# Performance work log

Measured on AMD Instinct MI355X. Metric: run time of the kernel, lower is better.

Reference implementation:

```python
import jax, jax.numpy as jnp
import numpy as np

NEG = -1000000.0  # mask fill value used by the torch module


def setup_inputs() -> dict:
    key = jax.random.key(0)
    kq, kk, kv, km = jax.random.split(key, 4)
    B, Q, K, D = 8, 2048, 2048, 128
    queries = jax.random.normal(kq, (B, Q, D), dtype=jnp.float32)
    keys = jax.random.normal(kk, (B, K, D), dtype=jnp.float32)
    values = jax.random.normal(kv, (B, K, D), dtype=jnp.float32)
    attntion_mask = jax.random.randint(km, (B, K), 0, 2, dtype=jnp.int32)
    return {"queries": queries, "keys": keys, "values": values,
            "attntion_mask": attntion_mask}


def reference(queries, keys, values, attntion_mask):
    d = queries.shape[-1]
    # scores: [B, Q, K]
    scores = jnp.einsum('bqd,bkd->bqk', queries, keys) / jnp.sqrt(
        jnp.asarray(d, dtype=queries.dtype))
    # 2D mask [B, K] broadcasts over the query axis (torch repeat_interleave)
    mask = attntion_mask.astype(bool)[:, None, :]  # [B, 1, K]
    scores = jnp.where(mask, scores, NEG)
    weights = jax.nn.softmax(scores, axis=-1)
    # dropout rate is 0.0 (eval mode) -> identity
    return jnp.einsum('bqk,bkv->bqv', weights, values)
```

## Files before the change

### kernel.cpp

```cpp
#include <hip/hip_runtime.h>
#include <stdint.h>

typedef __attribute__((ext_vector_type(8))) short short8;
typedef __attribute__((ext_vector_type(4))) float f32x4;

#define NB 8
#define NQ 2048
#define NK 2048
#define ND 128
#define SCALE 0.08838834764831845f
#define L2E   1.4426950408889634f
#define FMAXC 10.0f

__device__ __forceinline__ uint32_t pk_bf16(float a, float b) {
  uint32_t ua = __builtin_bit_cast(uint32_t, a);
  uint32_t ub = __builtin_bit_cast(uint32_t, b);
  ua += 0x7FFFu + ((ua >> 16) & 1u);
  ub += 0x7FFFu + ((ub >> 16) & 1u);
  return (ua >> 16) | (ub & 0xFFFF0000u);
}

__device__ __forceinline__ void dma16(const void* g, void* l) {
  __builtin_amdgcn_global_load_lds((const __attribute__((address_space(1))) void*)g,
                                   (__attribute__((address_space(3))) void*)l, 16, 0, 0);
}

__global__ __launch_bounds__(256) void compact_kernel(const int* __restrict__ maskm,
                                                      int* __restrict__ idxArr,
                                                      int* __restrict__ KcArr) {
  __shared__ int cnt;
  const int b = blockIdx.x;
  const int t = threadIdx.x;
  const int lane = t & 63;
  if (t == 0) cnt = 0;
  __syncthreads();
#pragma unroll
  for (int j = 0; j < 8; ++j) {
    int k = t * 8 + j;
    bool bit = maskm[b * NK + k] != 0;
    unsigned long long m = __ballot(bit);
    int pre = __popcll(m & ((1ull << lane) - 1ull));
    int tot = __popcll(m);
    int base = 0;
    if (lane == 0 && tot) base = atomicAdd(&cnt, tot);
    base = __shfl(base, 0);
    if (bit) idxArr[b * NK + base + pre] = k;
  }
  __syncthreads();
  int kc = cnt;
  for (int s = kc + t; s < NK; s += 256) idxArr[b * NK + s] = -1;
  if (t == 0) KcArr[b] = kc;
}

__global__ __launch_bounds__(256) void prep_kernel(const float* __restrict__ v,
                                                   const float* __restrict__ kin,
                                                   ushort* __restrict__ vt,
                                                   ushort* __restrict__ kb,
                                                   const int* __restrict__ idxArr) {
  const int t = threadIdx.x;
  const int bid = blockIdx.x;
  if (bid < 512) {
    __shared__ __align__(16) float tile[4096];
    char* sm = (char*)tile;
    const int b = bid >> 6;
    const int k0 = ((bid >> 1) & 31) << 6;
    const int d0 = (bid & 1) << 6;
#pragma unroll
    for (int i = 0; i < 4; ++i) {
      int id = i * 256 + t;
      int k = id >> 4, c = id & 15;
      int src = idxArr[b * NK + k0 + k];
      uint4 val; val.x = 0u; val.y = 0u; val.z = 0u; val.w = 0u;
      if (src >= 0) val = *(const uint4*)(v + (size_t)(b * NK + src) * ND + d0 + c * 4);
      *(uint4*)(sm + k * 256 + ((c ^ (k & 15)) * 16)) = val;
    }
    __syncthreads();
#pragma unroll
    for (int i = 0; i < 2; ++i) {
      int id = i * 256 + t;
      int d = id >> 3, kc = id & 7;
      uint32_t w[4];
#pragma unroll
      for (int jj = 0; jj < 4; ++jj) {
        int kA = kc * 8 + jj * 2, kB = kA + 1;
        float fa = *(const float*)(sm + kA * 256 + (((d >> 2) ^ (kA & 15)) * 16) + (d & 3) * 4);
        float fb = *(const float*)(sm + kB * 256 + (((d >> 2) ^ (kB & 15)) * 16) + (d & 3) * 4);
        w[jj] = pk_bf16(fa, fb);
      }
      uint4 o; o.x = w[0]; o.y = w[1]; o.z = w[2]; o.w = w[3];
      *(uint4*)(vt + (size_t)(b * ND + d0 + d) * NK + k0 + kc * 8) = o;
    }
  } else {
    int gs = (bid - 512) * 16 + (t >> 4);
    int src = idxArr[gs];
    int col = (t & 15) * 8;
    uint4 u; u.x = 0u; u.y = 0u; u.z = 0u; u.w = 0u;
    if (src >= 0) {
      int b2 = gs >> 11;
      const float* p = kin + (size_t)(b2 * NK + src) * ND + col;
      f32x4 a = *(const f32x4*)p;
      f32x4 c = *(const f32x4*)(p + 4);
      u.x = pk_bf16(a[0], a[1]); u.y = pk_bf16(a[2], a[3]);
      u.z = pk_bf16(c[0], c[1]); u.w = pk_bf16(c[2], c[3]);
    }
    *(uint4*)(kb + (size_t)gs * ND + col) = u;
  }
}

#define LDS_BYTES 73728
__global__ __launch_bounds__(256) void attn_kernel(const float* __restrict__ qm,
                                                   const ushort* __restrict__ kbm,
                                                   const ushort* __restrict__ vtm,
                                                   const int* __restrict__ KcArr,
                                                   ushort* __restrict__ opart,
                                                   float* __restrict__ lpart) {
  __shared__ __align__(16) char sm[LDS_BYTES];
  const int o   = blockIdx.x;
  const int bid = (o & 7) * 64 + (o >> 3);
  const int b   = bid >> 6;
  const int q0  = ((bid >> 1) & 31) << 6;
  const int spl = bid & 1;
  const int t = threadIdx.x;
  const int lane = t & 63;
  const int wave = t >> 6;
  const int r = lane & 15;
  const int quad = lane >> 4;
  const int half = wave >> 1;
  const int qg = wave & 1;

  const int Kc   = KcArr[b];
  const int n_it = (Kc + 127) >> 7;
  const int CH   = n_it << 5;

  uint32_t koff[4], voff[4];
#pragma unroll
  for (int j = 0; j < 4; ++j) {
    int i = wave * 4 + j;
    int rho = i * 4 + (lane >> 4);
    int ck = (lane & 15) ^ (rho & 15);
    int krow = (spl * 2 + (rho >> 5)) * CH + (rho & 31);
    koff[j] = (uint32_t)(b * NK + krow) * ND + ck * 8;
    int rv = i * 16 + (lane >> 2);
    int cv = (lane & 3) ^ (rv & 3);
    voff[j] = (uint32_t)(b * ND + (rv & 127)) * NK + (spl * 2 + (rv >> 7)) * CH + cv * 8;
  }

  short8 qf[2][4];
#pragma unroll
  for (int qt = 0; qt < 2; ++qt)
#pragma unroll
    for (int ks = 0; ks < 4; ++ks) {
      const float* p = qm + (size_t)(b * NQ + q0 + qg * 32 + qt * 16 + r) * ND + ks * 32 + quad * 8;
      f32x4 a = *(const f32x4*)p;
      f32x4 c = *(const f32x4*)(p + 4);
      uint4 u;
      u.x = pk_bf16(a[0], a[1]); u.y = pk_bf16(a[2], a[3]);
      u.z = pk_bf16(c[0], c[1]); u.w = pk_bf16(c[2], c[3]);
      qf[qt][ks] = __builtin_bit_cast(short8, u);
    }

  f32x4 oacc[2][8];
#pragma unroll
  for (int qt = 0; qt < 2; ++qt)
#pragma unroll
    for (int dt = 0; dt < 8; ++dt) oacc[qt][dt] = (f32x4){0.f, 0.f, 0.f, 0.f};
  float l_[2] = {0.f, 0.f};

  char* const pbase = sm + 65536 + wave * 2048;

  const int lim0 = Kc - (spl * 2 + half) * CH - quad * 4;

#pragma unroll
  for (int j = 0; j < 4; ++j) {
    dma16(kbm + koff[j], sm + wave * 4096 + j * 1024);
    dma16(vtm + voff[j], sm + 32768 + wave * 4096 + j * 1024);
  }

  for (int it = 0; it < n_it; ++it) {
    const int cur = it & 1;
    char* const kcur = sm + cur * 16384;
    char* const vcur = sm + 32768 + cur * 16384;
    char* const knxt = sm + (cur ^ 1) * 16384;
    char* const vnxt = sm + 32768 + (cur ^ 1) * 16384;

    __syncthreads();

    if (it < n_it - 1) {
      const uint32_t kadd = (uint32_t)(it + 1) * 32 * ND;
      const uint32_t vadd = (uint32_t)(it + 1) * 32;
#pragma unroll
      for (int j = 0; j < 4; ++j) {
        dma16(kbm + koff[j] + kadd, knxt + wave * 4096 + j * 1024);
        dma16(vtm + voff[j] + vadd, vnxt + wave * 4096 + j * 1024);
      }
    }

    short8 kf[2][4];
#pragma unroll
    for (int mt = 0; mt < 2; ++mt)
#pragma unroll
      for (int ks = 0; ks < 4; ++ks)
        kf[mt][ks] = *(const short8*)(kcur + half * 8192 + (mt * 16 + r) * 256 + (((ks * 4 + quad) ^ r) * 16));
    f32x4 st[2][2];
#pragma unroll
    for (int mt = 0; mt < 2; ++mt)
#pragma unroll
      for (int qt = 0; qt < 2; ++qt) {
        f32x4 acc = (f32x4){0.f, 0.f, 0.f, 0.f};
#pragma unroll
        for (int ks = 0; ks < 4; ++ks)
          acc = __builtin_amdgcn_mfma_f32_16x16x32_bf16(kf[mt][ks], qf[qt][ks], acc, 0, 0, 0);
        st[mt][qt] = acc;
      }

    const float C1 = SCALE * L2E;
    const float C2 = -FMAXC * L2E;
    const int rem = lim0 - it * 32;
#pragma unroll
    for (int qt = 0; qt < 2; ++qt) {
      float p[2][4]; float ps = 0.f;
#pragma unroll
      for (int mt = 0; mt < 2; ++mt) {
        const int rm = rem - mt * 16;
        float t0 = (rm > 0) ? fmaf(st[mt][qt][0], C1, C2) : -2.0e6f;
        float t1 = (rm > 1) ? fmaf(st[mt][qt][1], C1, C2) : -2.0e6f;
        float t2 = (rm > 2) ? fmaf(st[mt][qt][2], C1, C2) : -2.0e6f;
        float t3 = (rm > 3) ? fmaf(st[mt][qt][3], C1, C2) : -2.0e6f;
        p[mt][0] = exp2f(t0); p[mt][1] = exp2f(t1);
        p[mt][2] = exp2f(t2); p[mt][3] = exp2f(t3);
        ps += p[mt][0] + p[mt][1] + p[mt][2] + p[mt][3];
      }
      ps += __shfl_xor(ps, 16);
      ps += __shfl_xor(ps, 32);
      l_[qt] += ps;
#pragma unroll
      for (int mt = 0; mt < 2; ++mt) {
        uint2 w; w.x = pk_bf16(p[mt][0], p[mt][1]); w.y = pk_bf16(p[mt][2], p[mt][3]);
        *(uint2*)(pbase + (qt * 16 + r) * 64 + (((mt * 4 + quad) ^ (r & 6)) * 8)) = w;
      }
    }

    short8 pf[2];
#pragma unroll
    for (int qt = 0; qt < 2; ++qt)
      pf[qt] = *(const short8*)(pbase + (qt * 16 + r) * 64 + (((quad * 2) ^ (r & 6)) * 8));
#pragma unroll
    for (int dt = 0; dt < 8; ++dt) {
      short8 vf = *(const short8*)(vcur + half * 8192 + (dt * 16 + r) * 64 + ((quad ^ (r & 3)) * 16));
#pragma unroll
      for (int qt = 0; qt < 2; ++qt)
        oacc[qt][dt] = __builtin_amdgcn_mfma_f32_16x16x32_bf16(vf, pf[qt], oacc[qt][dt], 0, 0, 0);
    }
  }

  __syncthreads();
  float* xch = (float*)(sm + qg * 17408) + lane * 68;
  if (half == 1) {
    xch[0] = l_[0]; xch[1] = l_[1];
#pragma unroll
    for (int qt = 0; qt < 2; ++qt)
#pragma unroll
      for (int dt = 0; dt < 8; ++dt)
        *(f32x4*)(xch + 4 + (qt * 8 + dt) * 4) = oacc[qt][dt];
  }
  __syncthreads();
  if (half == 0) {
#pragma unroll
    for (int qt = 0; qt < 2; ++qt) {
      const int qrow = b * NQ + q0 + qg * 32 + qt * 16 + r;
      float lsum = l_[qt] + xch[qt];
      if (quad == 0) lpart[spl * NB * NQ + qrow] = lsum;
#pragma unroll
      for (int dt = 0; dt < 8; ++dt) {
        f32x4 o1 = *(const f32x4*)(xch + 4 + (qt * 8 + dt) * 4);
        f32x4 ov = oacc[qt][dt] + o1;
        uint2 w; w.x = pk_bf16(ov[0], ov[1]); w.y = pk_bf16(ov[2], ov[3]);
        *(uint2*)(opart + (size_t)spl * NB * NQ * ND + (size_t)qrow * ND + dt * 16 + quad * 4) = w;
      }
    }
  }
}

__global__ __launch_bounds__(256) void merge_kernel(const ushort* __restrict__ opart,
                                                    const float* __restrict__ lpart,
                                                    float* __restrict__ outm) {
  const int gid = blockIdx.x * 256 + threadIdx.x;
  const int row = gid >> 4;
  const int d0 = (gid & 15) << 3;
  const size_t off = (size_t)row * ND + d0;
  uint4 u0 = *(const uint4*)(opart + off);
  uint4 u1 = *(const uint4*)(opart + (size_t)NB * NQ * ND + off);
  float inv = 1.0f / (lpart[row] + lpart[NB * NQ + row]);
  f32x4 lo, hi;
  uint32_t w;
#define UP(u, dst0, dst1) w = (u); dst0 = __builtin_bit_cast(float, w << 16); \
                          dst1 = __builtin_bit_cast(float, w & 0xFFFF0000u);
  float a0,a1,b0,b1;
  UP(u0.x, a0, a1) UP(u1.x, b0, b1) lo[0] = (a0 + b0) * inv; lo[1] = (a1 + b1) * inv;
  UP(u0.y, a0, a1) UP(u1.y, b0, b1) lo[2] = (a0 + b0) * inv; lo[3] = (a1 + b1) * inv;
  UP(u0.z, a0, a1) UP(u1.z, b0, b1) hi[0] = (a0 + b0) * inv; hi[1] = (a1 + b1) * inv;
  UP(u0.w, a0, a1) UP(u1.w, b0, b1) hi[2] = (a0 + b0) * inv; hi[3] = (a1 + b1) * inv;
#undef UP
  *(f32x4*)(outm + off) = lo;
  *(f32x4*)(outm + off + 4) = hi;
}

extern "C" void kernel_launch(void* const* d_in, const int* in_sizes, int n_in,
                              void* d_out, int out_size, void* d_ws, size_t ws_size,
                              hipStream_t stream) {
  const float* q   = (const float*)d_in[0];
  const float* k   = (const float*)d_in[1];
  const float* v   = (const float*)d_in[2];
  const int*   msk = (const int*)d_in[3];
  float* out = (float*)d_out;
  ushort* kb = (ushort*)d_ws;
  ushort* vt = kb + (size_t)NB * NK * ND;
  ushort* op = vt + (size_t)NB * NK * ND;
  float*  lp = (float*)(op + 2 * (size_t)NB * NQ * ND);
  int* idxA  = (int*)(lp + 2 * (size_t)NB * NQ);
  int* kcA   = idxA + (size_t)NB * NK;

  compact_kernel<<<NB, 256, 0, stream>>>(msk, idxA, kcA);
  prep_kernel<<<1536, 256, 0, stream>>>(v, k, vt, kb, idxA);
  attn_kernel<<<512, 256, 0, stream>>>(q, kb, vt, kcA, op, lp);
  merge_kernel<<<1024, 256, 0, stream>>>(op, lp, out);
}
```

Baseline: 109.6 us.

## Fuse mask compaction into prep and load V fragments directly from global

New measurement: 113.4 us. +3.5%, slower.

```diff
diff --git a/kernel.cpp b/kernel.cpp
--- a/kernel.cpp
+++ b/kernel.cpp
@@ -25,51 +25,54 @@
                                    (__attribute__((address_space(3))) void*)l, 16, 0, 0);
 }
 
-__global__ __launch_bounds__(256) void compact_kernel(const int* __restrict__ maskm,
-                                                      int* __restrict__ idxArr,
-                                                      int* __restrict__ KcArr) {
-  __shared__ int cnt;
-  const int b = blockIdx.x;
-  const int t = threadIdx.x;
-  const int lane = t & 63;
-  if (t == 0) cnt = 0;
-  __syncthreads();
-#pragma unroll
-  for (int j = 0; j < 8; ++j) {
-    int k = t * 8 + j;
-    bool bit = maskm[b * NK + k] != 0;
-    unsigned long long m = __ballot(bit);
-    int pre = __popcll(m & ((1ull << lane) - 1ull));
-    int tot = __popcll(m);
-    int base = 0;
-    if (lane == 0 && tot) base = atomicAdd(&cnt, tot);
-    base = __shfl(base, 0);
-    if (bit) idxArr[b * NK + base + pre] = k;
-  }
-  __syncthreads();
-  int kc = cnt;
-  for (int s = kc + t; s < NK; s += 256) idxArr[b * NK + s] = -1;
-  if (t == 0) KcArr[b] = kc;
-}
-
 __global__ __launch_bounds__(256) void prep_kernel(const float* __restrict__ v,
                                                    const float* __restrict__ kin,
+                                                   const int* __restrict__ maskm,
                                                    ushort* __restrict__ vt,
                                                    ushort* __restrict__ kb,
-                                                   const int* __restrict__ idxArr) {
+                                                   int* __restrict__ KcArr) {
+  __shared__ int slotmap[NK];
+  __shared__ int wsum[4];
+  __shared__ __align__(16) float tile[4096];
   const int t = threadIdx.x;
   const int bid = blockIdx.x;
+  const int b = (bid < 512) ? (bid >> 6) : ((bid - 512) >> 4);
+  const int lane = t & 63;
+  const int wv = t >> 6;
+
+  int4 m0 = *(const int4*)(maskm + b * NK + t * 8);
+  int4 m1 = *(const int4*)(maskm + b * NK + t * 8 + 4);
+  int bits = (m0.x != 0) | ((m0.y != 0) << 1) | ((m0.z != 0) << 2) | ((m0.w != 0) << 3)
+           | ((m1.x != 0) << 4) | ((m1.y != 0) << 5) | ((m1.z != 0) << 6) | ((m1.w != 0) << 7);
+  int cnt = __popc(bits & 0xFF);
+  int pre = cnt;
+#pragma unroll
+  for (int d = 1; d < 64; d <<= 1) {
+    int x = __shfl_up(pre, d);
+    if (lane >= d) pre += x;
+  }
+  if (lane == 63) wsum[wv] = pre;
+  __syncthreads();
+  int base = pre - cnt;
+#pragma unroll
+  for (int w = 0; w < 4; ++w) if (w < wv) base += wsum[w];
+  const int Kc = wsum[0] + wsum[1] + wsum[2] + wsum[3];
+#pragma unroll
+  for (int j = 0; j < 8; ++j)
+    if ((bits >> j) & 1) slotmap[base++] = t * 8 + j;
+  for (int s = Kc + t; s < NK; s += 256) slotmap[s] = -1;
+  if (bid < 512 && (bid & 63) == 0 && t == 0) KcArr[b] = Kc;
+  __syncthreads();
+
   if (bid < 512) {
-    __shared__ __align__(16) float tile[4096];
     char* sm = (char*)tile;
-    const int b = bid >> 6;
     const int k0 = ((bid >> 1) & 31) << 6;
     const int d0 = (bid & 1) << 6;
 #pragma unroll
     for (int i = 0; i < 4; ++i) {
       int id = i * 256 + t;
       int k = id >> 4, c = id & 15;
-      int src = idxArr[b * NK + k0 + k];
+      int src = slotmap[k0 + k];
       uint4 val; val.x = 0u; val.y = 0u; val.z = 0u; val.w = 0u;
       if (src >= 0) val = *(const uint4*)(v + (size_t)(b * NK + src) * ND + d0 + c * 4);
       *(uint4*)(sm + k * 256 + ((c ^ (k & 15)) * 16)) = val;
@@ -91,23 +94,26 @@
       *(uint4*)(vt + (size_t)(b * ND + d0 + d) * NK + k0 + kc * 8) = o;
     }
   } else {
-    int gs = (bid - 512) * 16 + (t >> 4);
-    int src = idxArr[gs];
-    int col = (t & 15) * 8;
-    uint4 u; u.x = 0u; u.y = 0u; u.z = 0u; u.w = 0u;
-    if (src >= 0) {
-      int b2 = gs >> 11;
-      const float* p = kin + (size_t)(b2 * NK + src) * ND + col;
-      f32x4 a = *(const f32x4*)p;
-      f32x4 c = *(const f32x4*)(p + 4);
-      u.x = pk_bf16(a[0], a[1]); u.y = pk_bf16(a[2], a[3]);
-      u.z = pk_bf16(c[0], c[1]); u.w = pk_bf16(c[2], c[3]);
-    }
-    *(uint4*)(kb + (size_t)gs * ND + col) = u;
-  }
-}
-
-#define LDS_BYTES 73728
+    const int kblk = bid - 512;
+#pragma unroll
+    for (int pass = 0; pass < 8; ++pass) {
+      int slot = (kblk & 15) * 128 + pass * 16 + (t >> 4);
+      int src = slotmap[slot];
+      int col = (t & 15) * 8;
+      uint4 u; u.x = 0u; u.y = 0u; u.z = 0u; u.w = 0u;
+      if (src >= 0) {
+        const float* p = kin + (size_t)(b * NK + src) * ND + col;
+        f32x4 a = *(const f32x4*)p;
+        f32x4 c = *(const f32x4*)(p + 4);
+        u.x = pk_bf16(a[0], a[1]); u.y = pk_bf16(a[2], a[3]);
+        u.z = pk_bf16(c[0], c[1]); u.w = pk_bf16(c[2], c[3]);
+      }
+      *(uint4*)(kb + (size_t)(b * NK + slot) * ND + col) = u;
+    }
+  }
+}
+
+#define LDS_BYTES 40960
 __global__ __launch_bounds__(256) void attn_kernel(const float* __restrict__ qm,
                                                    const ushort* __restrict__ kbm,
                                                    const ushort* __restrict__ vtm,
@@ -132,7 +138,7 @@
   const int n_it = (Kc + 127) >> 7;
   const int CH   = n_it << 5;
 
-  uint32_t koff[4], voff[4];
+  uint32_t koff[4];
 #pragma unroll
   for (int j = 0; j < 4; ++j) {
     int i = wave * 4 + j;
@@ -140,10 +146,8 @@
     int ck = (lane & 15) ^ (rho & 15);
     int krow = (spl * 2 + (rho >> 5)) * CH + (rho & 31);
     koff[j] = (uint32_t)(b * NK + krow) * ND + ck * 8;
-    int rv = i * 16 + (lane >> 2);
-    int cv = (lane & 3) ^ (rv & 3);
-    voff[j] = (uint32_t)(b * ND + (rv & 127)) * NK + (spl * 2 + (rv >> 7)) * CH + cv * 8;
-  }
+  }
+  const ushort* vp0 = vtm + (size_t)(b * ND + r) * NK + (spl * 2 + half) * CH + quad * 8;
 
   short8 qf[2][4];
 #pragma unroll
@@ -166,33 +170,34 @@
     for (int dt = 0; dt < 8; ++dt) oacc[qt][dt] = (f32x4){0.f, 0.f, 0.f, 0.f};
   float l_[2] = {0.f, 0.f};
 
-  char* const pbase = sm + 65536 + wave * 2048;
+  char* const pbase = sm + 32768 + wave * 2048;
 
   const int lim0 = Kc - (spl * 2 + half) * CH - quad * 4;
 
 #pragma unroll
-  for (int j = 0; j < 4; ++j) {
+  for (int j = 0; j < 4; ++j)
     dma16(kbm + koff[j], sm + wave * 4096 + j * 1024);
-    dma16(vtm + voff[j], sm + 32768 + wave * 4096 + j * 1024);
-  }
 
   for (int it = 0; it < n_it; ++it) {
     const int cur = it & 1;
     char* const kcur = sm + cur * 16384;
-    char* const vcur = sm + 32768 + cur * 16384;
     char* const knxt = sm + (cur ^ 1) * 16384;
-    char* const vnxt = sm + 32768 + (cur ^ 1) * 16384;
 
     __syncthreads();
+
+    short8 vfr[8];
+    {
+      const ushort* vp = vp0 + it * 32;
+#pragma unroll
+      for (int dt = 0; dt < 8; ++dt)
+        vfr[dt] = *(const short8*)(vp + (size_t)dt * 16 * NK);
+    }
 
     if (it < n_it - 1) {
       const uint32_t kadd = (uint32_t)(it + 1) * 32 * ND;
-      const uint32_t vadd = (uint32_t)(it + 1) * 32;
-#pragma unroll
-      for (int j = 0; j < 4; ++j) {
+#pragma unroll
+      for (int j = 0; j < 4; ++j)
         dma16(kbm + koff[j] + kadd, knxt + wave * 4096 + j * 1024);
-        dma16(vtm + voff[j] + vadd, vnxt + wave * 4096 + j * 1024);
-      }
     }
 
     short8 kf[2][4];
@@ -246,10 +251,9 @@
       pf[qt] = *(const short8*)(pbase + (qt * 16 + r) * 64 + (((quad * 2) ^ (r & 6)) * 8));
 #pragma unroll
     for (int dt = 0; dt < 8; ++dt) {
-      short8 vf = *(const short8*)(vcur + half * 8192 + (dt * 16 + r) * 64 + ((quad ^ (r & 3)) * 16));
 #pragma unroll
       for (int qt = 0; qt < 2; ++qt)
-        oacc[qt][dt] = __builtin_amdgcn_mfma_f32_16x16x32_bf16(vf, pf[qt], oacc[qt][dt], 0, 0, 0);
+        oacc[qt][dt] = __builtin_amdgcn_mfma_f32_16x16x32_bf16(vfr[dt], pf[qt], oacc[qt][dt], 0, 0, 0);
     }
   }
 
@@ -317,11 +321,9 @@
   ushort* vt = kb + (size_t)NB * NK * ND;
   ushort* op = vt + (size_t)NB * NK * ND;
   float*  lp = (float*)(op + 2 * (size_t)NB * NQ * ND);
-  int* idxA  = (int*)(lp + 2 * (size_t)NB * NQ);
-  int* kcA   = idxA + (size_t)NB * NK;
-
-  compact_kernel<<<NB, 256, 0, stream>>>(msk, idxA, kcA);
-  prep_kernel<<<1536, 256, 0, stream>>>(v, k, vt, kb, idxA);
+  int* kcA   = (int*)(lp + 2 * (size_t)NB * NQ);
+
+  prep_kernel<<<640, 256, 0, stream>>>(v, k, msk, vt, kb, kcA);
   attn_kernel<<<512, 256, 0, stream>>>(q, kb, vt, kcA, op, lp);
   merge_kernel<<<1024, 256, 0, stream>>>(op, lp, out);
 }
```

## Fuse split-K merge into attention via atomic tickets, load V directly to registers

Applied to the files above, without the earlier changes.

Measured after the change: 186.8 us. 70.5% more time.

```diff
diff --git a/kernel.cpp b/kernel.cpp
--- a/kernel.cpp
+++ b/kernel.cpp
@@ -27,11 +27,13 @@
 
 __global__ __launch_bounds__(256) void compact_kernel(const int* __restrict__ maskm,
                                                       int* __restrict__ idxArr,
-                                                      int* __restrict__ KcArr) {
+                                                      int* __restrict__ KcArr,
+                                                      int* __restrict__ tkArr) {
   __shared__ int cnt;
   const int b = blockIdx.x;
   const int t = threadIdx.x;
   const int lane = t & 63;
+  if (t < 32) tkArr[b * 32 + t] = 0;
   if (t == 0) cnt = 0;
   __syncthreads();
 #pragma unroll
@@ -107,14 +109,51 @@
   }
 }
 
-#define LDS_BYTES 73728
+template <bool MASKED>
+__device__ __forceinline__ void do_softmax(const f32x4 st[2][2], float l_[2],
+                                           char* pbase, int r, int quad, int rem) {
+  const float C1 = SCALE * L2E;
+  const float C2 = -FMAXC * L2E;
+#pragma unroll
+  for (int qt = 0; qt < 2; ++qt) {
+    float p[2][4]; float ps = 0.f;
+#pragma unroll
+    for (int mt = 0; mt < 2; ++mt) {
+      float t0 = fmaf(st[mt][qt][0], C1, C2);
+      float t1 = fmaf(st[mt][qt][1], C1, C2);
+      float t2 = fmaf(st[mt][qt][2], C1, C2);
+      float t3 = fmaf(st[mt][qt][3], C1, C2);
+      if (MASKED) {
+        const int rm = rem - mt * 16;
+        t0 = (rm > 0) ? t0 : -2.0e6f;
+        t1 = (rm > 1) ? t1 : -2.0e6f;
+        t2 = (rm > 2) ? t2 : -2.0e6f;
+        t3 = (rm > 3) ? t3 : -2.0e6f;
+      }
+      p[mt][0] = exp2f(t0); p[mt][1] = exp2f(t1);
+      p[mt][2] = exp2f(t2); p[mt][3] = exp2f(t3);
+      ps += p[mt][0] + p[mt][1] + p[mt][2] + p[mt][3];
+    }
+    l_[qt] += ps;
+#pragma unroll
+    for (int mt = 0; mt < 2; ++mt) {
+      uint2 w; w.x = pk_bf16(p[mt][0], p[mt][1]); w.y = pk_bf16(p[mt][2], p[mt][3]);
+      *(uint2*)(pbase + (qt * 16 + r) * 64 + (((mt * 4 + quad) ^ (r & 6)) * 8)) = w;
+    }
+  }
+}
+
+#define LDS_BYTES 40960
 __global__ __launch_bounds__(256) void attn_kernel(const float* __restrict__ qm,
                                                    const ushort* __restrict__ kbm,
                                                    const ushort* __restrict__ vtm,
                                                    const int* __restrict__ KcArr,
                                                    ushort* __restrict__ opart,
-                                                   float* __restrict__ lpart) {
+                                                   float* __restrict__ lpart,
+                                                   float* __restrict__ outm,
+                                                   int* __restrict__ tkArr) {
   __shared__ __align__(16) char sm[LDS_BYTES];
+  __shared__ int tkS;
   const int o   = blockIdx.x;
   const int bid = (o & 7) * 64 + (o >> 3);
   const int b   = bid >> 6;
@@ -132,7 +171,7 @@
   const int n_it = (Kc + 127) >> 7;
   const int CH   = n_it << 5;
 
-  uint32_t koff[4], voff[4];
+  uint32_t koff[4];
 #pragma unroll
   for (int j = 0; j < 4; ++j) {
     int i = wave * 4 + j;
@@ -140,10 +179,12 @@
     int ck = (lane & 15) ^ (rho & 15);
     int krow = (spl * 2 + (rho >> 5)) * CH + (rho & 31);
     koff[j] = (uint32_t)(b * NK + krow) * ND + ck * 8;
-    int rv = i * 16 + (lane >> 2);
-    int cv = (lane & 3) ^ (rv & 3);
-    voff[j] = (uint32_t)(b * ND + (rv & 127)) * NK + (spl * 2 + (rv >> 7)) * CH + cv * 8;
-  }
+  }
+  const ushort* vp0 = vtm + (size_t)(b * ND + r) * NK + (spl * 2 + half) * CH + quad * 8;
+
+#pragma unroll
+  for (int j = 0; j < 4; ++j)
+    dma16(kbm + koff[j], sm + wave * 4096 + j * 1024);
 
   short8 qf[2][4];
 #pragma unroll
@@ -166,33 +207,30 @@
     for (int dt = 0; dt < 8; ++dt) oacc[qt][dt] = (f32x4){0.f, 0.f, 0.f, 0.f};
   float l_[2] = {0.f, 0.f};
 
-  char* const pbase = sm + 65536 + wave * 2048;
-
-  const int lim0 = Kc - (spl * 2 + half) * CH - quad * 4;
-
-#pragma unroll
-  for (int j = 0; j < 4; ++j) {
-    dma16(kbm + koff[j], sm + wave * 4096 + j * 1024);
-    dma16(vtm + voff[j], sm + 32768 + wave * 4096 + j * 1024);
-  }
+  char* const pbase = sm + 32768 + wave * 2048;
+
+  const int vlim0 = Kc - (spl * 2 + half) * CH;
 
   for (int it = 0; it < n_it; ++it) {
     const int cur = it & 1;
     char* const kcur = sm + cur * 16384;
-    char* const vcur = sm + 32768 + cur * 16384;
     char* const knxt = sm + (cur ^ 1) * 16384;
-    char* const vnxt = sm + 32768 + (cur ^ 1) * 16384;
 
     __syncthreads();
+
+    short8 vfr[8];
+    {
+      const ushort* vp = vp0 + it * 32;
+#pragma unroll
+      for (int dt = 0; dt < 8; ++dt)
+        vfr[dt] = *(const short8*)(vp + (size_t)dt * 16 * NK);
+    }
 
     if (it < n_it - 1) {
       const uint32_t kadd = (uint32_t)(it + 1) * 32 * ND;
-      const uint32_t vadd = (uint32_t)(it + 1) * 32;
-#pragma unroll
-      for (int j = 0; j < 4; ++j) {
+#pragma unroll
+      for (int j = 0; j < 4; ++j)
         dma16(kbm + koff[j] + kadd, knxt + wave * 4096 + j * 1024);
-        dma16(vtm + voff[j] + vadd, vnxt + wave * 4096 + j * 1024);
-      }
     }
 
     short8 kf[2][4];
@@ -213,32 +251,9 @@
         st[mt][qt] = acc;
       }
 
-    const float C1 = SCALE * L2E;
-    const float C2 = -FMAXC * L2E;
-    const int rem = lim0 - it * 32;
-#pragma unroll
-    for (int qt = 0; qt < 2; ++qt) {
-      float p[2][4]; float ps = 0.f;
-#pragma unroll
-      for (int mt = 0; mt < 2; ++mt) {
-        const int rm = rem - mt * 16;
-        float t0 = (rm > 0) ? fmaf(st[mt][qt][0], C1, C2) : -2.0e6f;
-        float t1 = (rm > 1) ? fmaf(st[mt][qt][1], C1, C2) : -2.0e6f;
-        float t2 = (rm > 2) ? fmaf(st[mt][qt][2], C1, C2) : -2.0e6f;
-        float t3 = (rm > 3) ? fmaf(st[mt][qt][3], C1, C2) : -2.0e6f;
-        p[mt][0] = exp2f(t0); p[mt][1] = exp2f(t1);
-        p[mt][2] = exp2f(t2); p[mt][3] = exp2f(t3);
-        ps += p[mt][0] + p[mt][1] + p[mt][2] + p[mt][3];
-      }
-      ps += __shfl_xor(ps, 16);
-      ps += __shfl_xor(ps, 32);
-      l_[qt] += ps;
-#pragma unroll
-      for (int mt = 0; mt < 2; ++mt) {
-        uint2 w; w.x = pk_bf16(p[mt][0], p[mt][1]); w.y = pk_bf16(p[mt][2], p[mt][3]);
-        *(uint2*)(pbase + (qt * 16 + r) * 64 + (((mt * 4 + quad) ^ (r & 6)) * 8)) = w;
-      }
-    }
+    const int vlim = vlim0 - it * 32;
+    if (vlim >= 32) do_softmax<false>(st, l_, pbase, r, quad, 0);
+    else            do_softmax<true >(st, l_, pbase, r, quad, vlim - quad * 4);
 
     short8 pf[2];
 #pragma unroll
@@ -246,10 +261,9 @@
       pf[qt] = *(const short8*)(pbase + (qt * 16 + r) * 64 + (((quad * 2) ^ (r & 6)) * 8));
 #pragma unroll
     for (int dt = 0; dt < 8; ++dt) {
-      short8 vf = *(const short8*)(vcur + half * 8192 + (dt * 16 + r) * 64 + ((quad ^ (r & 3)) * 16));
 #pragma unroll
       for (int qt = 0; qt < 2; ++qt)
-        oacc[qt][dt] = __builtin_amdgcn_mfma_f32_16x16x32_bf16(vf, pf[qt], oacc[qt][dt], 0, 0, 0);
+        oacc[qt][dt] = __builtin_amdgcn_mfma_f32_16x16x32_bf16(vfr[dt], pf[qt], oacc[qt][dt], 0, 0, 0);
     }
   }
 
@@ -264,12 +278,16 @@
         *(f32x4*)(xch + 4 + (qt * 8 + dt) * 4) = oacc[qt][dt];
   }
   __syncthreads();
+  float lsv[2] = {0.f, 0.f};
   if (half == 0) {
 #pragma unroll
     for (int qt = 0; qt < 2; ++qt) {
       const int qrow = b * NQ + q0 + qg * 32 + qt * 16 + r;
-      float lsum = l_[qt] + xch[qt];
-      if (quad == 0) lpart[spl * NB * NQ + qrow] = lsum;
+      float ls = l_[qt] + xch[qt];
+      ls += __shfl_xor(ls, 16);
+      ls += __shfl_xor(ls, 32);
+      lsv[qt] = ls;
+      if (quad == 0) lpart[spl * NB * NQ + qrow] = ls;
 #pragma unroll
       for (int dt = 0; dt < 8; ++dt) {
         f32x4 o1 = *(const f32x4*)(xch + 4 + (qt * 8 + dt) * 4);
@@ -279,30 +297,35 @@
       }
     }
   }
-}
-
-__global__ __launch_bounds__(256) void merge_kernel(const ushort* __restrict__ opart,
-                                                    const float* __restrict__ lpart,
-                                                    float* __restrict__ outm) {
-  const int gid = blockIdx.x * 256 + threadIdx.x;
-  const int row = gid >> 4;
-  const int d0 = (gid & 15) << 3;
-  const size_t off = (size_t)row * ND + d0;
-  uint4 u0 = *(const uint4*)(opart + off);
-  uint4 u1 = *(const uint4*)(opart + (size_t)NB * NQ * ND + off);
-  float inv = 1.0f / (lpart[row] + lpart[NB * NQ + row]);
-  f32x4 lo, hi;
-  uint32_t w;
-#define UP(u, dst0, dst1) w = (u); dst0 = __builtin_bit_cast(float, w << 16); \
-                          dst1 = __builtin_bit_cast(float, w & 0xFFFF0000u);
-  float a0,a1,b0,b1;
-  UP(u0.x, a0, a1) UP(u1.x, b0, b1) lo[0] = (a0 + b0) * inv; lo[1] = (a1 + b1) * inv;
-  UP(u0.y, a0, a1) UP(u1.y, b0, b1) lo[2] = (a0 + b0) * inv; lo[3] = (a1 + b1) * inv;
-  UP(u0.z, a0, a1) UP(u1.z, b0, b1) hi[0] = (a0 + b0) * inv; hi[1] = (a1 + b1) * inv;
-  UP(u0.w, a0, a1) UP(u1.w, b0, b1) hi[2] = (a0 + b0) * inv; hi[3] = (a1 + b1) * inv;
-#undef UP
-  *(f32x4*)(outm + off) = lo;
-  *(f32x4*)(outm + off + 4) = hi;
+  __threadfence();
+  __syncthreads();
+  if (t == 0) tkS = atomicAdd(tkArr + b * 32 + ((bid >> 1) & 31), 1);
+  __syncthreads();
+  if (tkS == 1 && half == 0) {
+    __threadfence();
+#pragma unroll
+    for (int qt = 0; qt < 2; ++qt) {
+      const int qrow = b * NQ + q0 + qg * 32 + qt * 16 + r;
+      float lo = *(const volatile float*)(lpart + (spl ^ 1) * NB * NQ + qrow);
+      float inv = 1.0f / (lsv[qt] + lo);
+#pragma unroll
+      for (int dt = 0; dt < 8; ++dt) {
+        f32x4 o1 = *(const f32x4*)(xch + 4 + (qt * 8 + dt) * 4);
+        f32x4 ov = oacc[qt][dt] + o1;
+        const volatile uint2* po = (const volatile uint2*)(opart +
+            (size_t)(spl ^ 1) * NB * NQ * ND + (size_t)qrow * ND + dt * 16 + quad * 4);
+        uint2 u; u.x = po->x; u.y = po->y;
+        float b0 = __builtin_bit_cast(float, u.x << 16);
+        float b1 = __builtin_bit_cast(float, u.x & 0xFFFF0000u);
+        float b2 = __builtin_bit_cast(float, u.y << 16);
+        float b3 = __builtin_bit_cast(float, u.y & 0xFFFF0000u);
+        f32x4 res;
+        res[0] = (ov[0] + b0) * inv; res[1] = (ov[1] + b1) * inv;
+        res[2] = (ov[2] + b2) * inv; res[3] = (ov[3] + b3) * inv;
+        *(f32x4*)(outm + (size_t)qrow * ND + dt * 16 + quad * 4) = res;
+      }
+    }
+  }
 }
 
 extern "C" void kernel_launch(void* const* d_in, const int* in_sizes, int n_in,
@@ -319,9 +342,9 @@
   float*  lp = (float*)(op + 2 * (size_t)NB * NQ * ND);
   int* idxA  = (int*)(lp + 2 * (size_t)NB * NQ);
   int* kcA   = idxA + (size_t)NB * NK;
-
-  compact_kernel<<<NB, 256, 0, stream>>>(msk, idxA, kcA);
+  int* tkA   = kcA + 64;
+
+  compact_kernel<<<NB, 256, 0, stream>>>(msk, idxA, kcA, tkA);
   prep_kernel<<<1536, 256, 0, stream>>>(v, k, vt, kb, idxA);
-  attn_kernel<<<512, 256, 0, stream>>>(q, kb, vt, kcA, op, lp);
-  merge_kernel<<<1024, 256, 0, stream>>>(op, lp, out);
-}
+  attn_kernel<<<512, 256, 0, stream>>>(q, kb, vt, kcA, op, lp, out, tkA);
+}
```

## Halve query tile, load V directly to registers, split masked softmax path

Applied to the files above, without the earlier changes.

Result: slower. 132.6 us (+21.0%).

```diff
diff --git a/kernel.cpp b/kernel.cpp
--- a/kernel.cpp
+++ b/kernel.cpp
@@ -107,18 +107,49 @@
   }
 }
 
-#define LDS_BYTES 73728
-__global__ __launch_bounds__(256) void attn_kernel(const float* __restrict__ qm,
-                                                   const ushort* __restrict__ kbm,
-                                                   const ushort* __restrict__ vtm,
-                                                   const int* __restrict__ KcArr,
-                                                   ushort* __restrict__ opart,
-                                                   float* __restrict__ lpart) {
+template <bool MASKED>
+__device__ __forceinline__ void do_softmax(const f32x4 st[2], float& l_,
+                                           char* pbase, int r, int quad, int rem) {
+  const float C1 = SCALE * L2E;
+  const float C2 = -FMAXC * L2E;
+  float p[2][4]; float ps = 0.f;
+#pragma unroll
+  for (int mt = 0; mt < 2; ++mt) {
+    float t0 = fmaf(st[mt][0], C1, C2);
+    float t1 = fmaf(st[mt][1], C1, C2);
+    float t2 = fmaf(st[mt][2], C1, C2);
+    float t3 = fmaf(st[mt][3], C1, C2);
+    if (MASKED) {
+      const int rm = rem - mt * 16;
+      t0 = (rm > 0) ? t0 : -2.0e6f;
+      t1 = (rm > 1) ? t1 : -2.0e6f;
+      t2 = (rm > 2) ? t2 : -2.0e6f;
+      t3 = (rm > 3) ? t3 : -2.0e6f;
+    }
+    p[mt][0] = exp2f(t0); p[mt][1] = exp2f(t1);
+    p[mt][2] = exp2f(t2); p[mt][3] = exp2f(t3);
+    ps += p[mt][0] + p[mt][1] + p[mt][2] + p[mt][3];
+  }
+  l_ += ps;
+#pragma unroll
+  for (int mt = 0; mt < 2; ++mt) {
+    uint2 w; w.x = pk_bf16(p[mt][0], p[mt][1]); w.y = pk_bf16(p[mt][2], p[mt][3]);
+    *(uint2*)(pbase + r * 64 + (((mt * 4 + quad) ^ (r & 6)) * 8)) = w;
+  }
+}
+
+#define LDS_BYTES 36864
+__global__ __launch_bounds__(256, 4) void attn_kernel(const float* __restrict__ qm,
+                                                      const ushort* __restrict__ kbm,
+                                                      const ushort* __restrict__ vtm,
+                                                      const int* __restrict__ KcArr,
+                                                      ushort* __restrict__ opart,
+                                                      float* __restrict__ lpart) {
   __shared__ __align__(16) char sm[LDS_BYTES];
   const int o   = blockIdx.x;
-  const int bid = (o & 7) * 64 + (o >> 3);
-  const int b   = bid >> 6;
-  const int q0  = ((bid >> 1) & 31) << 6;
+  const int bid = (o & 7) * 128 + (o >> 3);
+  const int b   = bid >> 7;
+  const int q0  = ((bid >> 1) & 63) << 5;
   const int spl = bid & 1;
   const int t = threadIdx.x;
   const int lane = t & 63;
@@ -132,7 +163,7 @@
   const int n_it = (Kc + 127) >> 7;
   const int CH   = n_it << 5;
 
-  uint32_t koff[4], voff[4];
+  uint32_t koff[4];
 #pragma unroll
   for (int j = 0; j < 4; ++j) {
     int i = wave * 4 + j;
@@ -140,59 +171,54 @@
     int ck = (lane & 15) ^ (rho & 15);
     int krow = (spl * 2 + (rho >> 5)) * CH + (rho & 31);
     koff[j] = (uint32_t)(b * NK + krow) * ND + ck * 8;
-    int rv = i * 16 + (lane >> 2);
-    int cv = (lane & 3) ^ (rv & 3);
-    voff[j] = (uint32_t)(b * ND + (rv & 127)) * NK + (spl * 2 + (rv >> 7)) * CH + cv * 8;
-  }
-
-  short8 qf[2][4];
-#pragma unroll
-  for (int qt = 0; qt < 2; ++qt)
-#pragma unroll
-    for (int ks = 0; ks < 4; ++ks) {
-      const float* p = qm + (size_t)(b * NQ + q0 + qg * 32 + qt * 16 + r) * ND + ks * 32 + quad * 8;
-      f32x4 a = *(const f32x4*)p;
-      f32x4 c = *(const f32x4*)(p + 4);
-      uint4 u;
-      u.x = pk_bf16(a[0], a[1]); u.y = pk_bf16(a[2], a[3]);
-      u.z = pk_bf16(c[0], c[1]); u.w = pk_bf16(c[2], c[3]);
-      qf[qt][ks] = __builtin_bit_cast(short8, u);
-    }
-
-  f32x4 oacc[2][8];
-#pragma unroll
-  for (int qt = 0; qt < 2; ++qt)
-#pragma unroll
-    for (int dt = 0; dt < 8; ++dt) oacc[qt][dt] = (f32x4){0.f, 0.f, 0.f, 0.f};
-  float l_[2] = {0.f, 0.f};
-
-  char* const pbase = sm + 65536 + wave * 2048;
-
-  const int lim0 = Kc - (spl * 2 + half) * CH - quad * 4;
-
-#pragma unroll
-  for (int j = 0; j < 4; ++j) {
+  }
+  const ushort* vp0 = vtm + (size_t)(b * ND + r) * NK + (spl * 2 + half) * CH + quad * 8;
+
+#pragma unroll
+  for (int j = 0; j < 4; ++j)
     dma16(kbm + koff[j], sm + wave * 4096 + j * 1024);
-    dma16(vtm + voff[j], sm + 32768 + wave * 4096 + j * 1024);
-  }
+
+  short8 qf[4];
+#pragma unroll
+  for (int ks = 0; ks < 4; ++ks) {
+    const float* p = qm + (size_t)(b * NQ + q0 + qg * 16 + r) * ND + ks * 32 + quad * 8;
+    f32x4 a = *(const f32x4*)p;
+    f32x4 c = *(const f32x4*)(p + 4);
+    uint4 u;
+    u.x = pk_bf16(a[0], a[1]); u.y = pk_bf16(a[2], a[3]);
+    u.z = pk_bf16(c[0], c[1]); u.w = pk_bf16(c[2], c[3]);
+    qf[ks] = __builtin_bit_cast(short8, u);
+  }
+
+  f32x4 oacc[8];
+#pragma unroll
+  for (int dt = 0; dt < 8; ++dt) oacc[dt] = (f32x4){0.f, 0.f, 0.f, 0.f};
+  float l_ = 0.f;
+
+  char* const pbase = sm + 32768 + wave * 1024;
+
+  const int vlim0 = Kc - (spl * 2 + half) * CH;
 
   for (int it = 0; it < n_it; ++it) {
     const int cur = it & 1;
     char* const kcur = sm + cur * 16384;
-    char* const vcur = sm + 32768 + cur * 16384;
     char* const knxt = sm + (cur ^ 1) * 16384;
-    char* const vnxt = sm + 32768 + (cur ^ 1) * 16384;
 
     __syncthreads();
+
+    short8 vfr[8];
+    {
+      const ushort* vp = vp0 + it * 32;
+#pragma unroll
+      for (int dt = 0; dt < 8; ++dt)
+        vfr[dt] = *(const short8*)(vp + (size_t)dt * 16 * NK);
+    }
 
     if (it < n_it - 1) {
       const uint32_t kadd = (uint32_t)(it + 1) * 32 * ND;
-      const uint32_t vadd = (uint32_t)(it + 1) * 32;
-#pragma unroll
-      for (int j = 0; j < 4; ++j) {
+#pragma unroll
+      for (int j = 0; j < 4; ++j)
         dma16(kbm + koff[j] + kadd, knxt + wave * 4096 + j * 1024);
-        dma16(vtm + voff[j] + vadd, vnxt + wave * 4096 + j * 1024);
-      }
     }
 
     short8 kf[2][4];
@@ -201,82 +227,47 @@
 #pragma unroll
       for (int ks = 0; ks < 4; ++ks)
         kf[mt][ks] = *(const short8*)(kcur + half * 8192 + (mt * 16 + r) * 256 + (((ks * 4 + quad) ^ r) * 16));
-    f32x4 st[2][2];
-#pragma unroll
-    for (int mt = 0; mt < 2; ++mt)
-#pragma unroll
-      for (int qt = 0; qt < 2; ++qt) {
-        f32x4 acc = (f32x4){0.f, 0.f, 0.f, 0.f};
-#pragma unroll
-        for (int ks = 0; ks < 4; ++ks)
-          acc = __builtin_amdgcn_mfma_f32_16x16x32_bf16(kf[mt][ks], qf[qt][ks], acc, 0, 0, 0);
-        st[mt][qt] = acc;
-      }
-
-    const float C1 = SCALE * L2E;
-    const float C2 = -FMAXC * L2E;
-    const int rem = lim0 - it * 32;
-#pragma unroll
-    for (int qt = 0; qt < 2; ++qt) {
-      float p[2][4]; float ps = 0.f;
-#pragma unroll
-      for (int mt = 0; mt < 2; ++mt) {
-        const int rm = rem - mt * 16;
-        float t0 = (rm > 0) ? fmaf(st[mt][qt][0], C1, C2) : -2.0e6f;
-        float t1 = (rm > 1) ? fmaf(st[mt][qt][1], C1, C2) : -2.0e6f;
-        float t2 = (rm > 2) ? fmaf(st[mt][qt][2], C1, C2) : -2.0e6f;
-        float t3 = (rm > 3) ? fmaf(st[mt][qt][3], C1, C2) : -2.0e6f;
-        p[mt][0] = exp2f(t0); p[mt][1] = exp2f(t1);
-        p[mt][2] = exp2f(t2); p[mt][3] = exp2f(t3);
-        ps += p[mt][0] + p[mt][1] + p[mt][2] + p[mt][3];
-      }
-      ps += __shfl_xor(ps, 16);
-      ps += __shfl_xor(ps, 32);
-      l_[qt] += ps;
-#pragma unroll
-      for (int mt = 0; mt < 2; ++mt) {
-        uint2 w; w.x = pk_bf16(p[mt][0], p[mt][1]); w.y = pk_bf16(p[mt][2], p[mt][3]);
-        *(uint2*)(pbase + (qt * 16 + r) * 64 + (((mt * 4 + quad) ^ (r & 6)) * 8)) = w;
-      }
-    }
-
-    short8 pf[2];
-#pragma unroll
-    for (int qt = 0; qt < 2; ++qt)
-      pf[qt] = *(const short8*)(pbase + (qt * 16 + r) * 64 + (((quad * 2) ^ (r & 6)) * 8));
-#pragma unroll
-    for (int dt = 0; dt < 8; ++dt) {
-      short8 vf = *(const short8*)(vcur + half * 8192 + (dt * 16 + r) * 64 + ((quad ^ (r & 3)) * 16));
-#pragma unroll
-      for (int qt = 0; qt < 2; ++qt)
-        oacc[qt][dt] = __builtin_amdgcn_mfma_f32_16x16x32_bf16(vf, pf[qt], oacc[qt][dt], 0, 0, 0);
-    }
+    f32x4 st[2];
+#pragma unroll
+    for (int mt = 0; mt < 2; ++mt) {
+      f32x4 acc = (f32x4){0.f, 0.f, 0.f, 0.f};
+#pragma unroll
+      for (int ks = 0; ks < 4; ++ks)
+        acc = __builtin_amdgcn_mfma_f32_16x16x32_bf16(kf[mt][ks], qf[ks], acc, 0, 0, 0);
+      st[mt] = acc;
+    }
+
+    const int vlim = vlim0 - it * 32;
+    if (vlim >= 32) do_softmax<false>(st, l_, pbase, r, quad, 0);
+    else            do_softmax<true >(st, l_, pbase, r, quad, vlim - quad * 4);
+
+    short8 pf = *(const short8*)(pbase + r * 64 + (((quad * 2) ^ (r & 6)) * 8));
+#pragma unroll
+    for (int dt = 0; dt < 8; ++dt)
+      oacc[dt] = __builtin_amdgcn_mfma_f32_16x16x32_bf16(vfr[dt], pf, oacc[dt], 0, 0, 0);
   }
 
   __syncthreads();
-  float* xch = (float*)(sm + qg * 17408) + lane * 68;
+  float* xch = (float*)(sm + qg * 9216) + lane * 36;
   if (half == 1) {
-    xch[0] = l_[0]; xch[1] = l_[1];
-#pragma unroll
-    for (int qt = 0; qt < 2; ++qt)
-#pragma unroll
-      for (int dt = 0; dt < 8; ++dt)
-        *(f32x4*)(xch + 4 + (qt * 8 + dt) * 4) = oacc[qt][dt];
+    xch[0] = l_;
+#pragma unroll
+    for (int dt = 0; dt < 8; ++dt)
+      *(f32x4*)(xch + 4 + dt * 4) = oacc[dt];
   }
   __syncthreads();
   if (half == 0) {
-#pragma unroll
-    for (int qt = 0; qt < 2; ++qt) {
-      const int qrow = b * NQ + q0 + qg * 32 + qt * 16 + r;
-      float lsum = l_[qt] + xch[qt];
-      if (quad == 0) lpart[spl * NB * NQ + qrow] = lsum;
-#pragma unroll
-      for (int dt = 0; dt < 8; ++dt) {
-        f32x4 o1 = *(const f32x4*)(xch + 4 + (qt * 8 + dt) * 4);
-        f32x4 ov = oacc[qt][dt] + o1;
-        uint2 w; w.x = pk_bf16(ov[0], ov[1]); w.y = pk_bf16(ov[2], ov[3]);
-        *(uint2*)(opart + (size_t)spl * NB * NQ * ND + (size_t)qrow * ND + dt * 16 + quad * 4) = w;
-      }
+    const int qrow = b * NQ + q0 + qg * 16 + r;
+    float ls = l_ + xch[0];
+    ls += __shfl_xor(ls, 16);
+    ls += __shfl_xor(ls, 32);
+    if (quad == 0) lpart[spl * NB * NQ + qrow] = ls;
+#pragma unroll
+    for (int dt = 0; dt < 8; ++dt) {
+      f32x4 o1 = *(const f32x4*)(xch + 4 + dt * 4);
+      f32x4 ov = oacc[dt] + o1;
+      uint2 w; w.x = pk_bf16(ov[0], ov[1]); w.y = pk_bf16(ov[2], ov[3]);
+      *(uint2*)(opart + (size_t)spl * NB * NQ * ND + (size_t)qrow * ND + dt * 16 + quad * 4) = w;
     }
   }
 }
@@ -322,6 +313,6 @@
 
   compact_kernel<<<NB, 256, 0, stream>>>(msk, idxA, kcA);
   prep_kernel<<<1536, 256, 0, stream>>>(v, k, vt, kb, idxA);
-  attn_kernel<<<512, 256, 0, stream>>>(q, kb, vt, kcA, op, lp);
+  attn_kernel<<<1024, 256, 0, stream>>>(q, kb, vt, kcA, op, lp);
   merge_kernel<<<1024, 256, 0, stream>>>(op, lp, out);
 }
```
